# Optimization experiments

Hardware: AMD Instinct MI355X
Metric: run time of the kernel (lower is better)

## Reference

```python
import jax, jax.numpy as jnp
import numpy as np

N_GRAPHS = 100
NODES_PER_GRAPH = 1000
N = N_GRAPHS * NODES_PER_GRAPH
DEG = 16
E = N * DEG
IN_FEATS = 64
HIDDEN = 128
READOUT_DIM = HIDDEN // 2
SLOPE = 0.01
EPS = 1e-5


def leaky(x):
    return jnp.where(x >= 0, x, SLOPE * x)


def _kaiming(k, shape):
    # torch kaiming_uniform_, fan_in mode, leaky_relu gain
    fan_in = shape[0]
    gain = np.sqrt(2.0 / (1.0 + SLOPE ** 2))
    bound = gain * np.sqrt(3.0 / fan_in)
    return jax.random.uniform(k, shape, jnp.float32, -bound, bound)


def setup_inputs() -> dict:
    key = jax.random.key(0)
    ks = jax.random.split(key, 16)
    node_feats = jax.random.normal(ks[0], (N, IN_FEATS), jnp.float32)
    # within-graph random edges (batched graph of equal-sized components)
    src_local = jax.random.randint(ks[1], (E,), 0, NODES_PER_GRAPH)
    dst_local = jax.random.randint(ks[2], (E,), 0, NODES_PER_GRAPH)
    edge_graph = jnp.repeat(jnp.arange(N_GRAPHS, dtype=jnp.int32), E // N_GRAPHS)
    src = (edge_graph * NODES_PER_GRAPH + src_local).astype(jnp.int32)
    dst = (edge_graph * NODES_PER_GRAPH + dst_local).astype(jnp.int32)
    edge_weights = jax.random.uniform(ks[3], (E,), jnp.float32)
    node_graph = jnp.repeat(jnp.arange(N_GRAPHS, dtype=jnp.int32), NODES_PER_GRAPH)
    return {
        "node_feats": node_feats,
        "edge_weights": edge_weights,
        "W1": _kaiming(ks[4], (IN_FEATS, HIDDEN)),
        "W2": _kaiming(ks[5], (HIDDEN, HIDDEN)),
        "gn1_alpha": jnp.ones((HIDDEN,), jnp.float32),
        "gn1_gamma": jnp.ones((HIDDEN,), jnp.float32),
        "gn1_beta": jnp.zeros((HIDDEN,), jnp.float32),
        "gn2_alpha": jnp.ones((HIDDEN,), jnp.float32),
        "gn2_gamma": jnp.ones((HIDDEN,), jnp.float32),
        "gn2_beta": jnp.zeros((HIDDEN,), jnp.float32),
        "r1_w1": _kaiming(ks[6], (HIDDEN, HIDDEN)),
        "r1_b1": jnp.zeros((HIDDEN,), jnp.float32),
        "r1_w2": _kaiming(ks[7], (HIDDEN, READOUT_DIM)),
        "r1_b2": jnp.zeros((READOUT_DIM,), jnp.float32),
        "r2_w1": _kaiming(ks[8], (HIDDEN, HIDDEN)),
        "r2_b1": jnp.zeros((HIDDEN,), jnp.float32),
        "r2_w2": _kaiming(ks[9], (HIDDEN, READOUT_DIM)),
        "r2_b2": jnp.zeros((READOUT_DIM,), jnp.float32),
        "src": src,
        "dst": dst,
        "node_graph": node_graph,
    }


def _graph_conv(x, W, src, dst, ew, out_isqrt, in_isqrt):
    # DGL GraphConv norm='both', no bias: D_in^{-1/2} A_w D_out^{-1/2} X W
    h = (x * out_isqrt[:, None]) @ W                 # [N, out]
    m = h[src] * ew[:, None]                         # [E, out] gather + edge weight
    agg = jax.ops.segment_sum(m, dst, num_segments=N)  # scatter-add
    return agg * in_isqrt[:, None]


def _graph_norm(x, alpha, gamma, beta, node_graph, inv_cnt):
    mean = jax.ops.segment_sum(x, node_graph, num_segments=N_GRAPHS) * inv_cnt
    sub = x - alpha * mean[node_graph]
    var = jax.ops.segment_sum(sub * sub, node_graph, num_segments=N_GRAPHS) * inv_cnt
    return gamma * sub / jnp.sqrt(var[node_graph] + EPS) + beta


def _readout(x, w1, b1, w2, b2, node_graph, inv_cnt):
    # deep-sets style universal readout: rho(mean(phi(h_v)))
    h = leaky(x @ w1 + b1)
    pooled = jax.ops.segment_sum(h, node_graph, num_segments=N_GRAPHS) * inv_cnt
    return leaky(pooled @ w2 + b2)


def reference(node_feats, edge_weights, W1, W2,
              gn1_alpha, gn1_gamma, gn1_beta,
              gn2_alpha, gn2_gamma, gn2_beta,
              r1_w1, r1_b1, r1_w2, r1_b2,
              r2_w1, r2_b1, r2_w2, r2_b2,
              src, dst, node_graph):
    ones_e = jnp.ones((E,), jnp.float32)
    out_deg = jnp.clip(jax.ops.segment_sum(ones_e, src, num_segments=N), 1.0)
    in_deg = jnp.clip(jax.ops.segment_sum(ones_e, dst, num_segments=N), 1.0)
    out_isqrt = jax.lax.rsqrt(out_deg)
    in_isqrt = jax.lax.rsqrt(in_deg)
    inv_cnt = 1.0 / NODES_PER_GRAPH

    h = _graph_conv(node_feats, W1, src, dst, edge_weights, out_isqrt, in_isqrt)
    h = leaky(_graph_norm(h, gn1_alpha, gn1_gamma, gn1_beta, node_graph, inv_cnt))
    # dropout is identity in eval mode
    r1 = _readout(h, r1_w1, r1_b1, r1_w2, r1_b2, node_graph, inv_cnt)
    m1 = jax.ops.segment_sum(h, node_graph, num_segments=N_GRAPHS) * inv_cnt

    h = _graph_conv(h, W2, src, dst, edge_weights, out_isqrt, in_isqrt)
    h = leaky(_graph_norm(h, gn2_alpha, gn2_gamma, gn2_beta, node_graph, inv_cnt))
    r2 = _readout(h, r2_w1, r2_b1, r2_w2, r2_b2, node_graph, inv_cnt)
    m2 = jax.ops.segment_sum(h, node_graph, num_segments=N_GRAPHS) * inv_cnt

    readout = jnp.concatenate([r1, m1, r2, m2], axis=1)  # [G, 2*H + 2*H/2] = [100, 384]
    return leaky(readout)
```

## Files before the change

kernel.cpp:

```cpp
#include <hip/hip_runtime.h>
#include <cstddef>
#include <cstdint>

#define NG   100
#define NPG  1000
#define NN   (NG * NPG)
#define NE   (NN * 16)
#define EPG  (NE / NG)
#define CSRG 40000
#define MINREC 20
#define FIN  64
#define HID  128
#define RD   64
#define SLOPE 0.01f
#define EPSV  1e-5f
#define NSTRIP 250
#define GSN   40

using short8 = __attribute__((ext_vector_type(8))) short;
using f32x4  = __attribute__((ext_vector_type(4))) float;
typedef unsigned short u16;

__device__ __forceinline__ float leaky(float x) { return x >= 0.f ? x : SLOPE * x; }

__device__ __forceinline__ u16 f2bf(float f) {
  union { float f; unsigned u; } v; v.f = f;
  return (u16)((v.u + 0x7fffu + ((v.u >> 16) & 1u)) >> 16);
}
__device__ __forceinline__ float bf2f(u16 u) {
  union { unsigned u; float f; } v; v.u = ((unsigned)u) << 16;
  return v.f;
}

__device__ __forceinline__ bool swz(int b, int per_g, int& g, int& part) {
  const int xcd = b & 7;
  const int slot = b >> 3;
  g = xcd + 8 * (slot / per_g);
  part = slot % per_g;
  return g < NG;
}

__global__ __launch_bounds__(256) void wt_k(const float* __restrict__ W1,
                                            const float* __restrict__ W2,
                                            const float* __restrict__ R1,
                                            const float* __restrict__ R2,
                                            u16* __restrict__ Wt1,
                                            u16* __restrict__ Wt2,
                                            u16* __restrict__ Rt1,
                                            u16* __restrict__ Rt2) {
  const int idx = blockIdx.x * 256 + threadIdx.x;
  if (idx < FIN * HID) {
    const int n = idx >> 6, k = idx & 63;
    Wt1[idx] = f2bf(W1[k * HID + n]);
  } else {
    const int j = idx - FIN * HID;
    const int m = j >> 14, r = j & 16383;
    const int n = r >> 7, k = r & 127;
    const float* s = (m == 0) ? W2 : (m == 1) ? R1 : R2;
    u16* d = (m == 0) ? Wt2 : (m == 1) ? Rt1 : Rt2;
    d[r] = f2bf(s[k * HID + n]);
  }
}

__global__ __launch_bounds__(1024) void build_k(const int* __restrict__ src,
                                                const int* __restrict__ dst,
                                                const float* __restrict__ ew,
                                                int* __restrict__ cin_,
                                                int* __restrict__ cout_,
                                                int* __restrict__ offs,
                                                unsigned* __restrict__ csr) {
  __shared__ int hin[NPG];
  __shared__ int hout[NPG];
  __shared__ int cur[NPG];
  __shared__ int wtot[16];
  int g, part;
  if (!swz(blockIdx.x, 1, g, part)) return;
  const int t = threadIdx.x;
  const int lane = t & 63, wave = t >> 6;
  const int nb = g * NPG, eb = g * EPG;
  if (t < NPG) { hin[t] = 0; hout[t] = 0; }
  __syncthreads();
  for (int e = t; e < EPG; e += 4096) {
    int s4[4], d4[4];
#pragma unroll
    for (int k = 0; k < 4; ++k) {
      const int ee = e + k * 1024;
      if (ee < EPG) { s4[k] = src[eb + ee]; d4[k] = dst[eb + ee]; }
      else d4[k] = -1;
    }
#pragma unroll
    for (int k = 0; k < 4; ++k)
      if (d4[k] >= 0) {
        atomicAdd(&hout[s4[k] - nb], 1);
        atomicAdd(&hin[d4[k] - nb], 1);
      }
  }
  __syncthreads();
  int v[4], vr[4];
  int loc = 0;
#pragma unroll
  for (int k = 0; k < 4; ++k) {
    const int idx = t * 4 + k;
    v[k] = (idx < NPG) ? hin[idx] : 0;
    const int c4 = (v[k] + 3) & ~3;
    vr[k] = (idx < NPG) ? ((c4 > MINREC) ? c4 : MINREC) : 0;
    loc += vr[k];
  }
  int incl = loc;
#pragma unroll
  for (int d = 1; d < 64; d <<= 1) {
    const int x = __shfl_up(incl, d);
    if (lane >= d) incl += x;
  }
  if (lane == 63) wtot[wave] = incl;
  if (t < NPG) { cin_[nb + t] = hin[t]; cout_[nb + t] = hout[t]; }
  __syncthreads();
  int wexc = 0;
  for (int i = 0; i < wave; ++i) wexc += wtot[i];
  int run = g * CSRG + wexc + (incl - loc);
#pragma unroll
  for (int k = 0; k < 4; ++k) {
    const int idx = t * 4 + k;
    if (idx < NPG) {
      offs[nb + idx] = run;
      cur[idx] = run;
      for (int z = v[k]; z < vr[k]; ++z) csr[run + z] = 0;
      run += vr[k];
    }
  }
  __syncthreads();
  for (int e = t; e < EPG; e += 4096) {
    int s4[4], d4[4]; float w4[4];
#pragma unroll
    for (int k = 0; k < 4; ++k) {
      const int ee = e + k * 1024;
      if (ee < EPG) { s4[k] = src[eb + ee]; d4[k] = dst[eb + ee]; w4[k] = ew[eb + ee]; }
      else d4[k] = -1;
    }
#pragma unroll
    for (int k = 0; k < 4; ++k)
      if (d4[k] >= 0) {
        const int pos = atomicAdd(&cur[d4[k] - nb], 1);
        csr[pos] = ((unsigned)(s4[k] - nb) << 16) | (unsigned)f2bf(w4[k]);
      }
  }
}

__global__ __launch_bounds__(256) void gemm1_k(const float* __restrict__ X,
                                               const u16* __restrict__ Wt,
                                               const int* __restrict__ cout_,
                                               u16* __restrict__ Y) {
  __shared__ u16 Xl[64 * FIN];
  __shared__ u16 Wl[HID * FIN];
  const int tid = threadIdx.x;
  const int wave = tid >> 6, lane = tid & 63, l15 = lane & 15, quad = lane >> 4;
  int g, part;
  if (!swz(blockIdx.x, 4, g, part)) return;
  const int base = g * NPG + part * NSTRIP;
  const int kq = tid & 15;
  const int srow = tid >> 4;

  for (int i = tid; i < HID * (FIN / 8); i += 256) {
    const int n = i >> 3, c = i & 7;
    const short8 w = *(const short8*)(Wt + n * FIN + c * 8);
    *(short8*)&Wl[n * FIN + ((c ^ (n & 7)) << 3)] = w;
  }
  float4 xpre[4];
#pragma unroll
  for (int it = 0; it < 4; ++it) {
    const int rowi = srow + it * 16;
    xpre[it] = (rowi < NSTRIP) ? *(const float4*)(X + (size_t)(base + rowi) * FIN + kq * 4)
                               : make_float4(0.f, 0.f, 0.f, 0.f);
  }
  for (int pass = 0; pass < 4; ++pass) {
    __syncthreads();
#pragma unroll
    for (int it = 0; it < 4; ++it) {
      const int r = srow + it * 16;
      ushort4 u = make_ushort4(f2bf(xpre[it].x), f2bf(xpre[it].y),
                               f2bf(xpre[it].z), f2bf(xpre[it].w));
      const int c = kq >> 1, half = kq & 1;
      *(ushort4*)&Xl[r * FIN + (((c ^ (r & 7)) << 3) | (half << 2))] = u;
    }
    __syncthreads();
    if (pass < 3) {
#pragma unroll
      for (int it = 0; it < 4; ++it) {
        const int rowi = (pass + 1) * 64 + srow + it * 16;
        xpre[it] = (rowi < NSTRIP) ? *(const float4*)(X + (size_t)(base + rowi) * FIN + kq * 4)
                                   : make_float4(0.f, 0.f, 0.f, 0.f);
      }
    }
    short8 a[2];
    const int arow = wave * 16 + l15;
#pragma unroll
    for (int kt = 0; kt < 2; ++kt)
      a[kt] = *(const short8*)&Xl[arow * FIN + (((kt * 4 + quad) ^ (l15 & 7)) << 3)];
    float sc[4];
    int rows[4];
#pragma unroll
    for (int r = 0; r < 4; ++r) {
      rows[r] = pass * 64 + wave * 16 + quad * 4 + r;
      sc[r] = (rows[r] < NSTRIP) ? rsqrtf(fmaxf((float)cout_[base + rows[r]], 1.0f)) : 0.f;
    }
#pragma unroll
    for (int ct = 0; ct < 8; ++ct) {
      f32x4 acc = {0.f, 0.f, 0.f, 0.f};
      const int brow = ct * 16 + l15;
#pragma unroll
      for (int kt = 0; kt < 2; ++kt) {
        const short8 b = *(const short8*)&Wl[brow * FIN + (((kt * 4 + quad) ^ (l15 & 7)) << 3)];
        acc = __builtin_amdgcn_mfma_f32_16x16x32_bf16(a[kt], b, acc, 0, 0, 0);
      }
      const int n = ct * 16 + l15;
#pragma unroll
      for (int r = 0; r < 4; ++r)
        if (rows[r] < NSTRIP) Y[(size_t)(base + rows[r]) * HID + n] = f2bf(acc[r] * sc[r]);
    }
  }
}

__device__ __forceinline__ void norm_affine(const float* sx, const float* sq,
                                            const float* alpha, const float* gamma,
                                            const float* beta, int g, int c8,
                                            float* Av, float* Bv) {
  const float inv = 1.0f / NPG;
#pragma unroll
  for (int j = 0; j < 8; ++j) {
    const int f = c8 * 8 + j;
    const float mean = sx[g * HID + f] * inv;
    const float ex2 = sq[g * HID + f] * inv;
    const float am = alpha[f] * mean;
    const float var = fmaxf(ex2 - 2.0f * am * mean + am * am, 0.0f);
    const float A = gamma[f] * rsqrtf(var + EPSV);
    Av[j] = A;
    Bv[j] = beta[f] - A * am;
  }
}

__global__ __launch_bounds__(256) void gemm_norm_k(const u16* __restrict__ Xb,
                                                   const u16* __restrict__ Wt,
                                                   const float* __restrict__ sx,
                                                   const float* __restrict__ sq,
                                                   const float* __restrict__ alpha,
                                                   const float* __restrict__ gamma,
                                                   const float* __restrict__ beta,
                                                   const int* __restrict__ cout_,
                                                   u16* __restrict__ Y) {
  __shared__ u16 Xl[64 * HID];
  __shared__ u16 Wl[HID * HID];
  const int tid = threadIdx.x;
  const int wave = tid >> 6, lane = tid & 63, l15 = lane & 15, quad = lane >> 4;
  int g, part;
  if (!swz(blockIdx.x, 4, g, part)) return;
  const int base = g * NPG + part * NSTRIP;
  const int c8 = tid & 15;
  const int srow = tid >> 4;

  for (int i = tid; i < HID * (HID / 8); i += 256) {
    const int n = i >> 4, c = i & 15;
    const short8 w = *(const short8*)(Wt + n * HID + c * 8);
    *(short8*)&Wl[n * HID + ((c ^ (n & 15)) << 3)] = w;
  }
  float Av[8], Bv[8];
  norm_affine(sx, sq, alpha, gamma, beta, g, c8, Av, Bv);
  const short8 z8 = {0, 0, 0, 0, 0, 0, 0, 0};
  short8 xpre[4];
#pragma unroll
  for (int it = 0; it < 4; ++it) {
    const int rowi = srow + it * 16;
    xpre[it] = (rowi < NSTRIP) ? *(const short8*)(Xb + (size_t)(base + rowi) * HID + c8 * 8) : z8;
  }
  for (int pass = 0; pass < 4; ++pass) {
    __syncthreads();
#pragma unroll
    for (int it = 0; it < 4; ++it) {
      const int r = srow + it * 16;
      const int rowi = pass * 64 + r;
      short8 o = z8;
      if (rowi < NSTRIP) {
#pragma unroll
        for (int j = 0; j < 8; ++j)
          o[j] = (short)f2bf(leaky(fmaf(Av[j], bf2f((u16)xpre[it][j]), Bv[j])));
      }
      *(short8*)&Xl[r * HID + ((c8 ^ (r & 15)) << 3)] = o;
    }
    __syncthreads();
    if (pass < 3) {
#pragma unroll
      for (int it = 0; it < 4; ++it) {
        const int rowi = (pass + 1) * 64 + srow + it * 16;
        xpre[it] = (rowi < NSTRIP) ? *(const short8*)(Xb + (size_t)(base + rowi) * HID + c8 * 8) : z8;
      }
    }
    short8 a[4];
    const int arow = wave * 16 + l15;
#pragma unroll
    for (int kt = 0; kt < 4; ++kt)
      a[kt] = *(const short8*)&Xl[arow * HID + (((kt * 4 + quad) ^ l15) << 3)];
    float sc[4];
    int rows[4];
#pragma unroll
    for (int r = 0; r < 4; ++r) {
      rows[r] = pass * 64 + wave * 16 + quad * 4 + r;
      sc[r] = (rows[r] < NSTRIP) ? rsqrtf(fmaxf((float)cout_[base + rows[r]], 1.0f)) : 0.f;
    }
#pragma unroll
    for (int ct = 0; ct < 8; ++ct) {
      f32x4 acc = {0.f, 0.f, 0.f, 0.f};
      const int brow = ct * 16 + l15;
#pragma unroll
      for (int kt = 0; kt < 4; ++kt) {
        const short8 b = *(const short8*)&Wl[brow * HID + (((kt * 4 + quad) ^ l15) << 3)];
        acc = __builtin_amdgcn_mfma_f32_16x16x32_bf16(a[kt], b, acc, 0, 0, 0);
      }
      const int n = ct * 16 + l15;
#pragma unroll
      for (int r = 0; r < 4; ++r)
        if (rows[r] < NSTRIP) Y[(size_t)(base + rows[r]) * HID + n] = f2bf(acc[r] * sc[r]);
    }
  }
}

struct RedT { float red[16][HID]; float hred[16][HID]; };
union ShT { u16 Xl[64 * HID]; RedT r; };

__global__ __launch_bounds__(256) void phi_pool_k(const u16* __restrict__ Xb,
                                                  const float* __restrict__ sx,
                                                  const float* __restrict__ sq,
                                                  const float* __restrict__ alpha,
                                                  const float* __restrict__ gamma,
                                                  const float* __restrict__ beta,
                                                  const u16* __restrict__ Wt,
                                                  const float* __restrict__ b1,
                                                  float* __restrict__ phi_sum,
                                                  float* __restrict__ h_sum) {
  __shared__ ShT sh;
  __shared__ u16 Wl[HID * HID];
  const int tid = threadIdx.x;
  const int wave = tid >> 6, lane = tid & 63, l15 = lane & 15, quad = lane >> 4;
  int g, part;
  if (!swz(blockIdx.x, 4, g, part)) return;
  const int base = g * NPG + part * NSTRIP;
  const int c8 = tid & 15;
  const int srow = tid >> 4;

  for (int i = tid; i < HID * (HID / 8); i += 256) {
    const int n = i >> 4, c = i & 15;
    const short8 w = *(const short8*)(Wt + n * HID + c * 8);
    *(short8*)&Wl[n * HID + ((c ^ (n & 15)) << 3)] = w;
  }
  float Av[8], Bv[8];
  norm_affine(sx, sq, alpha, gamma, beta, g, c8, Av, Bv);
  float bcol[8];
#pragma unroll
  for (int ct = 0; ct < 8; ++ct) bcol[ct] = b1[ct * 16 + l15];

  float pooled[8] = {0.f, 0.f, 0.f, 0.f, 0.f, 0.f, 0.f, 0.f};
  float hp[8] = {0.f, 0.f, 0.f, 0.f, 0.f, 0.f, 0.f, 0.f};
  const short8 z8 = {0, 0, 0, 0, 0, 0, 0, 0};
  short8 xpre[4];
#pragma unroll
  for (int it = 0; it < 4; ++it) {
    const int rowi = srow + it * 16;
    xpre[it] = (rowi < NSTRIP) ? *(const short8*)(Xb + (size_t)(base + rowi) * HID + c8 * 8) : z8;
  }
  for (int pass = 0; pass < 4; ++pass) {
    __syncthreads();
#pragma unroll
    for (int it = 0; it < 4; ++it) {
      const int r = srow + it * 16;
      const int rowi = pass * 64 + r;
      short8 o = z8;
      if (rowi < NSTRIP) {
#pragma unroll
        for (int j = 0; j < 8; ++j) {
          const float xn = leaky(fmaf(Av[j], bf2f((u16)xpre[it][j]), Bv[j]));
          hp[j] += xn;
          o[j] = (short)f2bf(xn);
        }
      }
      *(short8*)&sh.Xl[r * HID + ((c8 ^ (r & 15)) << 3)] = o;
    }
    __syncthreads();
    if (pass < 3) {
#pragma unroll
      for (int it = 0; it < 4; ++it) {
        const int rowi = (pass + 1) * 64 + srow + it * 16;
        xpre[it] = (rowi < NSTRIP) ? *(const short8*)(Xb + (size_t)(base + rowi) * HID + c8 * 8) : z8;
      }
    }
    short8 a[4];
    const int arow = wave * 16 + l15;
#pragma unroll
    for (int kt = 0; kt < 4; ++kt)
      a[kt] = *(const short8*)&sh.Xl[arow * HID + (((kt * 4 + quad) ^ l15) << 3)];
#pragma unroll
    for (int ct = 0; ct < 8; ++ct) {
      f32x4 acc = {0.f, 0.f, 0.f, 0.f};
      const int brow = ct * 16 + l15;
#pragma unroll
      for (int kt = 0; kt < 4; ++kt) {
        const short8 b = *(const short8*)&Wl[brow * HID + (((kt * 4 + quad) ^ l15) << 3)];
        acc = __builtin_amdgcn_mfma_f32_16x16x32_bf16(a[kt], b, acc, 0, 0, 0);
      }
#pragma unroll
      for (int r = 0; r < 4; ++r) {
        const int rowi = pass * 64 + wave * 16 + quad * 4 + r;
        if (rowi < NSTRIP) pooled[ct] += leaky(acc[r] + bcol[ct]);
      }
    }
  }
  __syncthreads();
  const int qi = wave * 4 + quad;
#pragma unroll
  for (int ct = 0; ct < 8; ++ct) sh.r.red[qi][ct * 16 + l15] = pooled[ct];
#pragma unroll
  for (int j = 0; j < 8; ++j) sh.r.hred[tid >> 4][(tid & 15) * 8 + j] = hp[j];
  __syncthreads();
  if (tid < HID) {
    float s = 0.f;
#pragma unroll
    for (int q = 0; q < 16; ++q) s += sh.r.red[q][tid];
    unsafeAtomicAdd(&phi_sum[g * HID + tid], s);
  } else {
    const int t = tid - HID;
    float s = 0.f;
#pragma unroll
    for (int rr = 0; rr < 16; ++rr) s += sh.r.hred[rr][t];
    unsafeAtomicAdd(&h_sum[g * HID + t], s);
  }
}

__global__ __launch_bounds__(256) void gather_k(const u16* __restrict__ H,
                                                const unsigned* __restrict__ csr,
                                                const int* __restrict__ offs,
                                                const int* __restrict__ cin_,
                                                u16* __restrict__ AGG,
                                                float* __restrict__ sx,
                                                float* __restrict__ sq) {
  __shared__ float redx[4][HID];
  __shared__ float redq[4][HID];
  const int wave = threadIdx.x >> 6;
  const int lane = threadIdx.x & 63;
  int g, part;
  if (!swz(blockIdx.x, 25, g, part)) return;
  const int nb = g * NPG;
  const int base = nb + part * GSN;
  const int loff = lane * 2;
  const u16* __restrict__ Hg = H + (size_t)nb * HID;

  float sxa = 0.f, sxb = 0.f, sqa = 0.f, sqb = 0.f;
  for (int it = 0; it < 3; ++it) {
    const int nc = (it < 2) ? 4 : 2;
    int nn[4], off[4], cnt[4], c4p[4];
    float isq[4];
    const uint4* p[4];
#pragma unroll
    for (int c = 0; c < 4; ++c) {
      const int j = it * 4 + c;
      const int node = base + wave + ((j < 10) ? j : 0) * 4;
      nn[c] = node;
      const int nu = __builtin_amdgcn_readfirstlane(node);
      off[c] = __builtin_amdgcn_readfirstlane(offs[nu]);
      cnt[c] = (c < nc) ? __builtin_amdgcn_readfirstlane(cin_[nu]) : 0;
      const int cr = (cnt[c] + 3) & ~3;
      c4p[c] = ((cr > MINREC) ? cr : MINREC) >> 2;
      isq[c] = rsqrtf(fmaxf((float)cnt[c], 1.0f));
      p[c] = (const uint4*)__builtin_assume_aligned(csr + off[c], 16);
    }
    float ax[4] = {0.f, 0.f, 0.f, 0.f};
    float ay[4] = {0.f, 0.f, 0.f, 0.f};
#pragma unroll
    for (int t = 0; t < 5; ++t) {
      uint4 r[4];
      unsigned u[4][4];
#pragma unroll
      for (int c = 0; c < 4; ++c)
        if (c < nc) {
          r[c] = p[c][t];
          u[c][0] = *(const unsigned*)(Hg + (size_t)(r[c].x >> 16) * HID + loff);
          u[c][1] = *(const unsigned*)(Hg + (size_t)(r[c].y >> 16) * HID + loff);
          u[c][2] = *(const unsigned*)(Hg + (size_t)(r[c].z >> 16) * HID + loff);
          u[c][3] = *(const unsigned*)(Hg + (size_t)(r[c].w >> 16) * HID + loff);
        }
#pragma unroll
      for (int c = 0; c < 4; ++c)
        if (c < nc) {
          const float w0 = bf2f((u16)(r[c].x & 0xffffu));
          const float w1 = bf2f((u16)(r[c].y & 0xffffu));
          const float w2 = bf2f((u16)(r[c].z & 0xffffu));
          const float w3 = bf2f((u16)(r[c].w & 0xffffu));
          ax[c] = fmaf(w0, __uint_as_float(u[c][0] << 16), ax[c]);
          ay[c] = fmaf(w0, __uint_as_float(u[c][0] & 0xffff0000u), ay[c]);
          ax[c] = fmaf(w1, __uint_as_float(u[c][1] << 16), ax[c]);
          ay[c] = fmaf(w1, __uint_as_float(u[c][1] & 0xffff0000u), ay[c]);
          ax[c] = fmaf(w2, __uint_as_float(u[c][2] << 16), ax[c]);
          ay[c] = fmaf(w2, __uint_as_float(u[c][2] & 0xffff0000u), ay[c]);
          ax[c] = fmaf(w3, __uint_as_float(u[c][3] << 16), ax[c]);
          ay[c] = fmaf(w3, __uint_as_float(u[c][3] & 0xffff0000u), ay[c]);
        }
    }
#pragma unroll
    for (int c = 0; c < 4; ++c) {
      for (int t = 5; t < c4p[c]; ++t) {
        const uint4 r = p[c][t];
        const unsigned u0 = *(const unsigned*)(Hg + (size_t)(r.x >> 16) * HID + loff);
        const unsigned u1 = *(const unsigned*)(Hg + (size_t)(r.y >> 16) * HID + loff);
        const unsigned u2 = *(const unsigned*)(Hg + (size_t)(r.z >> 16) * HID + loff);
        const unsigned u3 = *(const unsigned*)(Hg + (size_t)(r.w >> 16) * HID + loff);
        const float w0 = bf2f((u16)(r.x & 0xffffu));
        const float w1 = bf2f((u16)(r.y & 0xffffu));
        const float w2 = bf2f((u16)(r.z & 0xffffu));
        const float w3 = bf2f((u16)(r.w & 0xffffu));
        ax[c] = fmaf(w0, __uint_as_float(u0 << 16), ax[c]);
        ay[c] = fmaf(w0, __uint_as_float(u0 & 0xffff0000u), ay[c]);
        ax[c] = fmaf(w1, __uint_as_float(u1 << 16), ax[c]);
        ay[c] = fmaf(w1, __uint_as_float(u1 & 0xffff0000u), ay[c]);
        ax[c] = fmaf(w2, __uint_as_float(u2 << 16), ax[c]);
        ay[c] = fmaf(w2, __uint_as_float(u2 & 0xffff0000u), ay[c]);
        ax[c] = fmaf(w3, __uint_as_float(u3 << 16), ax[c]);
        ay[c] = fmaf(w3, __uint_as_float(u3 & 0xffff0000u), ay[c]);
      }
    }
#pragma unroll
    for (int c = 0; c < 4; ++c)
      if (c < nc) {
        const float rx = ax[c] * isq[c];
        const float ry = ay[c] * isq[c];
        *(unsigned*)(AGG + (size_t)nn[c] * HID + loff) =
            (unsigned)f2bf(rx) | ((unsigned)f2bf(ry) << 16);
        sxa += rx; sxb += ry;
        sqa += rx * rx; sqb += ry * ry;
      }
  }
  redx[wave][loff] = sxa; redx[wave][loff + 1] = sxb;
  redq[wave][loff] = sqa; redq[wave][loff + 1] = sqb;
  __syncthreads();
  const int tid = threadIdx.x;
  if (tid < HID) {
    unsafeAtomicAdd(&sx[g * HID + tid],
                    redx[0][tid] + redx[1][tid] + redx[2][tid] + redx[3][tid]);
  } else {
    const int t = tid - HID;
    unsafeAtomicAdd(&sq[g * HID + t],
                    redq[0][t] + redq[1][t] + redq[2][t] + redq[3][t]);
  }
}

__global__ __launch_bounds__(64) void finalize_k(const float* __restrict__ phi_sum,
                                                 const float* __restrict__ h_sum,
                                                 const float* __restrict__ w2,
                                                 const float* __restrict__ b2,
                                                 float* __restrict__ out,
                                                 int roff, int moff) {
  const int g = blockIdx.x;
  const int j = threadIdx.x;
  float acc = b2[j];
#pragma unroll 8
  for (int k = 0; k < HID; ++k)
    acc += (phi_sum[g * HID + k] * (1.0f / NPG)) * w2[k * RD + j];
  const float r = leaky(acc);
  out[g * 384 + roff + j] = leaky(r);
  out[g * 384 + moff + j] = leaky(h_sum[g * HID + j] * (1.0f / NPG));
  out[g * 384 + moff + 64 + j] = leaky(h_sum[g * HID + 64 + j] * (1.0f / NPG));
}

extern "C" void kernel_launch(void* const* d_in, const int* in_sizes, int n_in,
                              void* d_out, int out_size, void* d_ws, size_t ws_size,
                              hipStream_t stream) {
  const float* node_feats = (const float*)d_in[0];
  const float* ew   = (const float*)d_in[1];
  const float* W1   = (const float*)d_in[2];
  const float* W2   = (const float*)d_in[3];
  const float* g1a  = (const float*)d_in[4];
  const float* g1g  = (const float*)d_in[5];
  const float* g1b  = (const float*)d_in[6];
  const float* g2a  = (const float*)d_in[7];
  const float* g2g  = (const float*)d_in[8];
  const float* g2b  = (const float*)d_in[9];
  const float* r1w1 = (const float*)d_in[10];
  const float* r1b1 = (const float*)d_in[11];
  const float* r1w2 = (const float*)d_in[12];
  const float* r1b2 = (const float*)d_in[13];
  const float* r2w1 = (const float*)d_in[14];
  const float* r2b1 = (const float*)d_in[15];
  const float* r2w2 = (const float*)d_in[16];
  const float* r2b2 = (const float*)d_in[17];
  const int* src = (const int*)d_in[18];
  const int* dst = (const int*)d_in[19];
  float* out = (float*)d_out;

  char* wsb = (char*)d_ws;
  float* ps1     = (float*)wsb;
  float* hs1     = ps1 + NG * HID;
  float* ps2     = hs1 + NG * HID;
  float* hs2     = ps2 + NG * HID;
  float* sx1     = hs2 + NG * HID;
  float* sq1     = sx1 + NG * HID;
  float* sx2     = sq1 + NG * HID;
  float* sq2     = sx2 + NG * HID;
  int*   cin     = (int*)(sq2 + NG * HID);
  int*   cout_   = cin + NN;
  int*   offs    = cout_ + NN;
  unsigned* csr  = (unsigned*)(offs + NN);
  u16*   Wt1     = (u16*)(csr + (size_t)NG * CSRG);
  u16*   Wt2     = Wt1 + HID * FIN;
  u16*   Rt1     = Wt2 + HID * HID;
  u16*   Rt2     = Rt1 + HID * HID;
  u16*   bufA    = Rt2 + HID * HID;
  u16*   bufB    = bufA + (size_t)NN * HID;

  hipMemsetAsync(d_ws, 0, (size_t)(8 * NG * HID) * sizeof(float), stream);

  wt_k<<<(FIN * HID + 3 * HID * HID) / 256, 256, 0, stream>>>(
      W1, W2, r1w1, r2w1, Wt1, Wt2, Rt1, Rt2);
  build_k<<<8 * 13, 1024, 0, stream>>>(src, dst, ew, cin, cout_, offs, csr);

  const int gemm_grid = 8 * 4 * 13;
  const int gather_grid = 8 * 25 * 13;

  gemm1_k<<<gemm_grid, 256, 0, stream>>>(node_feats, Wt1, cout_, bufA);
  gather_k<<<gather_grid, 256, 0, stream>>>(bufA, csr, offs, cin, bufB, sx1, sq1);
  phi_pool_k<<<gemm_grid, 256, 0, stream>>>(bufB, sx1, sq1, g1a, g1g, g1b,
                                            Rt1, r1b1, ps1, hs1);
  finalize_k<<<NG, 64, 0, stream>>>(ps1, hs1, r1w2, r1b2, out, 0, 64);

  gemm_norm_k<<<gemm_grid, 256, 0, stream>>>(bufB, Wt2, sx1, sq1, g1a, g1g, g1b,
                                             cout_, bufA);
  gather_k<<<gather_grid, 256, 0, stream>>>(bufA, csr, offs, cin, bufB, sx2, sq2);
  phi_pool_k<<<gemm_grid, 256, 0, stream>>>(bufB, sx2, sq2, g2a, g2g, g2b,
                                            Rt2, r2b1, ps2, hs2);
  finalize_k<<<NG, 64, 0, stream>>>(ps2, hs2, r2w2, r2b2, out, 192, 256);
}
```

Before: 294.2 us.

## Fuse preprocessing, CSR build and first GEMM into one front kernel; merge phi-pool with next GEMM

```diff
diff --git a/kernel.cpp b/kernel.cpp
--- a/kernel.cpp
+++ b/kernel.cpp
@@ -40,182 +40,166 @@
   return g < NG;
 }
 
-__global__ __launch_bounds__(256) void wt_k(const float* __restrict__ W1,
-                                            const float* __restrict__ W2,
-                                            const float* __restrict__ R1,
-                                            const float* __restrict__ R2,
-                                            u16* __restrict__ Wt1,
-                                            u16* __restrict__ Wt2,
-                                            u16* __restrict__ Rt1,
-                                            u16* __restrict__ Rt2) {
-  const int idx = blockIdx.x * 256 + threadIdx.x;
-  if (idx < FIN * HID) {
-    const int n = idx >> 6, k = idx & 63;
-    Wt1[idx] = f2bf(W1[k * HID + n]);
-  } else {
-    const int j = idx - FIN * HID;
-    const int m = j >> 14, r = j & 16383;
-    const int n = r >> 7, k = r & 127;
-    const float* s = (m == 0) ? W2 : (m == 1) ? R1 : R2;
-    u16* d = (m == 0) ? Wt2 : (m == 1) ? Rt1 : Rt2;
-    d[r] = f2bf(s[k * HID + n]);
-  }
-}
-
-__global__ __launch_bounds__(1024) void build_k(const int* __restrict__ src,
-                                                const int* __restrict__ dst,
-                                                const float* __restrict__ ew,
-                                                int* __restrict__ cin_,
-                                                int* __restrict__ cout_,
-                                                int* __restrict__ offs,
-                                                unsigned* __restrict__ csr) {
-  __shared__ int hin[NPG];
-  __shared__ int hout[NPG];
-  __shared__ int cur[NPG];
-  __shared__ int wtot[16];
+struct BldSh { int hin[NPG]; int hout[NPG]; int cur[NPG]; int wtot[16]; };
+struct GemSh { u16 Xl[64 * FIN]; u16 W[HID * FIN]; };
+union FrontSh { BldSh b; GemSh g; };
+
+__global__ __launch_bounds__(1024) void front_k(
+    const float* __restrict__ X0, const float* __restrict__ ew,
+    const int* __restrict__ src, const int* __restrict__ dst,
+    const float* __restrict__ W1, const float* __restrict__ W2f,
+    const float* __restrict__ R1f, const float* __restrict__ R2f,
+    u16* __restrict__ Wt2, u16* __restrict__ Rt1, u16* __restrict__ Rt2,
+    int* __restrict__ cin_, int* __restrict__ offs,
+    unsigned* __restrict__ csr, u16* __restrict__ bufA,
+    float* __restrict__ zeroreg) {
+  __shared__ FrontSh u;
+  const int b = blockIdx.x;
+  const int t = threadIdx.x;
+  if (b >= 208) {
+    const int idx = (b - 208) * 1024 + t;
+    if (idx < 3 * HID * HID) {
+      const int m = idx >> 14, r = idx & 16383;
+      const int n = r >> 7, k = r & 127;
+      const float* s = (m == 0) ? W2f : (m == 1) ? R1f : R2f;
+      u16* d = (m == 0) ? Wt2 : (m == 1) ? Rt1 : Rt2;
+      d[r] = f2bf(s[k * HID + n]);
+    }
+    if (idx < (8 * NG * HID) / 4)
+      ((float4*)zeroreg)[idx] = make_float4(0.f, 0.f, 0.f, 0.f);
+    return;
+  }
   int g, part;
-  if (!swz(blockIdx.x, 1, g, part)) return;
-  const int t = threadIdx.x;
+  if (!swz(b, 2, g, part)) return;
   const int lane = t & 63, wave = t >> 6;
   const int nb = g * NPG, eb = g * EPG;
-  if (t < NPG) { hin[t] = 0; hout[t] = 0; }
-  __syncthreads();
-  for (int e = t; e < EPG; e += 4096) {
-    int s4[4], d4[4];
+
+  if (part == 0) {
+    if (t < NPG) { u.b.hin[t] = 0; u.b.hout[t] = 0; }
+    __syncthreads();
+    for (int e = t; e < EPG; e += 4096) {
+      int s4[4], d4[4];
+#pragma unroll
+      for (int k = 0; k < 4; ++k) {
+        const int ee = e + k * 1024;
+        if (ee < EPG) { s4[k] = src[eb + ee]; d4[k] = dst[eb + ee]; }
+        else d4[k] = -1;
+      }
+#pragma unroll
+      for (int k = 0; k < 4; ++k)
+        if (d4[k] >= 0) {
+          atomicAdd(&u.b.hout[s4[k] - nb], 1);
+          atomicAdd(&u.b.hin[d4[k] - nb], 1);
+        }
+    }
+    __syncthreads();
+    float* houtf = (float*)u.b.hout;
+    if (t < NPG) {
+      const int c = u.b.hout[t];
+      houtf[t] = rsqrtf((float)(c > 0 ? c : 1));
+    }
+    int v[4], vr[4];
+    int loc = 0;
 #pragma unroll
     for (int k = 0; k < 4; ++k) {
-      const int ee = e + k * 1024;
-      if (ee < EPG) { s4[k] = src[eb + ee]; d4[k] = dst[eb + ee]; }
-      else d4[k] = -1;
-    }
-#pragma unroll
-    for (int k = 0; k < 4; ++k)
-      if (d4[k] >= 0) {
-        atomicAdd(&hout[s4[k] - nb], 1);
-        atomicAdd(&hin[d4[k] - nb], 1);
-      }
-  }
-  __syncthreads();
-  int v[4], vr[4];
-  int loc = 0;
-#pragma unroll
-  for (int k = 0; k < 4; ++k) {
-    const int idx = t * 4 + k;
-    v[k] = (idx < NPG) ? hin[idx] : 0;
-    const int c4 = (v[k] + 3) & ~3;
-    vr[k] = (idx < NPG) ? ((c4 > MINREC) ? c4 : MINREC) : 0;
-    loc += vr[k];
-  }
-  int incl = loc;
-#pragma unroll
-  for (int d = 1; d < 64; d <<= 1) {
-    const int x = __shfl_up(incl, d);
-    if (lane >= d) incl += x;
-  }
-  if (lane == 63) wtot[wave] = incl;
-  if (t < NPG) { cin_[nb + t] = hin[t]; cout_[nb + t] = hout[t]; }
-  __syncthreads();
-  int wexc = 0;
-  for (int i = 0; i < wave; ++i) wexc += wtot[i];
-  int run = g * CSRG + wexc + (incl - loc);
-#pragma unroll
-  for (int k = 0; k < 4; ++k) {
-    const int idx = t * 4 + k;
-    if (idx < NPG) {
-      offs[nb + idx] = run;
-      cur[idx] = run;
-      for (int z = v[k]; z < vr[k]; ++z) csr[run + z] = 0;
-      run += vr[k];
-    }
-  }
-  __syncthreads();
-  for (int e = t; e < EPG; e += 4096) {
-    int s4[4], d4[4]; float w4[4];
+      const int idx = t * 4 + k;
+      v[k] = (idx < NPG) ? u.b.hin[idx] : 0;
+      const int c4 = (v[k] + 3) & ~3;
+      vr[k] = (idx < NPG) ? ((c4 > MINREC) ? c4 : MINREC) : 0;
+      loc += vr[k];
+    }
+    int incl = loc;
+#pragma unroll
+    for (int d = 1; d < 64; d <<= 1) {
+      const int x = __shfl_up(incl, d);
+      if (lane >= d) incl += x;
+    }
+    if (lane == 63) u.b.wtot[wave] = incl;
+    if (t < NPG) cin_[nb + t] = u.b.hin[t];
+    __syncthreads();
+    int wexc = 0;
+    for (int i = 0; i < wave; ++i) wexc += u.b.wtot[i];
+    int run = g * CSRG + wexc + (incl - loc);
 #pragma unroll
     for (int k = 0; k < 4; ++k) {
-      const int ee = e + k * 1024;
-      if (ee < EPG) { s4[k] = src[eb + ee]; d4[k] = dst[eb + ee]; w4[k] = ew[eb + ee]; }
-      else d4[k] = -1;
-    }
-#pragma unroll
-    for (int k = 0; k < 4; ++k)
-      if (d4[k] >= 0) {
-        const int pos = atomicAdd(&cur[d4[k] - nb], 1);
-        csr[pos] = ((unsigned)(s4[k] - nb) << 16) | (unsigned)f2bf(w4[k]);
-      }
-  }
-}
-
-__global__ __launch_bounds__(256) void gemm1_k(const float* __restrict__ X,
-                                               const u16* __restrict__ Wt,
-                                               const int* __restrict__ cout_,
-                                               u16* __restrict__ Y) {
-  __shared__ u16 Xl[64 * FIN];
-  __shared__ u16 Wl[HID * FIN];
-  const int tid = threadIdx.x;
-  const int wave = tid >> 6, lane = tid & 63, l15 = lane & 15, quad = lane >> 4;
-  int g, part;
-  if (!swz(blockIdx.x, 4, g, part)) return;
-  const int base = g * NPG + part * NSTRIP;
-  const int kq = tid & 15;
-  const int srow = tid >> 4;
-
-  for (int i = tid; i < HID * (FIN / 8); i += 256) {
-    const int n = i >> 3, c = i & 7;
-    const short8 w = *(const short8*)(Wt + n * FIN + c * 8);
-    *(short8*)&Wl[n * FIN + ((c ^ (n & 7)) << 3)] = w;
-  }
-  float4 xpre[4];
-#pragma unroll
-  for (int it = 0; it < 4; ++it) {
-    const int rowi = srow + it * 16;
-    xpre[it] = (rowi < NSTRIP) ? *(const float4*)(X + (size_t)(base + rowi) * FIN + kq * 4)
-                               : make_float4(0.f, 0.f, 0.f, 0.f);
-  }
-  for (int pass = 0; pass < 4; ++pass) {
+      const int idx = t * 4 + k;
+      if (idx < NPG) {
+        offs[nb + idx] = run;
+        u.b.cur[idx] = run;
+        for (int z = v[k]; z < vr[k]; ++z) csr[run + z] = 0;
+        run += vr[k];
+      }
+    }
     __syncthreads();
-#pragma unroll
-    for (int it = 0; it < 4; ++it) {
-      const int r = srow + it * 16;
-      ushort4 u = make_ushort4(f2bf(xpre[it].x), f2bf(xpre[it].y),
-                               f2bf(xpre[it].z), f2bf(xpre[it].w));
-      const int c = kq >> 1, half = kq & 1;
-      *(ushort4*)&Xl[r * FIN + (((c ^ (r & 7)) << 3) | (half << 2))] = u;
-    }
-    __syncthreads();
-    if (pass < 3) {
-#pragma unroll
-      for (int it = 0; it < 4; ++it) {
-        const int rowi = (pass + 1) * 64 + srow + it * 16;
-        xpre[it] = (rowi < NSTRIP) ? *(const float4*)(X + (size_t)(base + rowi) * FIN + kq * 4)
-                                   : make_float4(0.f, 0.f, 0.f, 0.f);
-      }
-    }
-    short8 a[2];
-    const int arow = wave * 16 + l15;
-#pragma unroll
-    for (int kt = 0; kt < 2; ++kt)
-      a[kt] = *(const short8*)&Xl[arow * FIN + (((kt * 4 + quad) ^ (l15 & 7)) << 3)];
-    float sc[4];
-    int rows[4];
-#pragma unroll
-    for (int r = 0; r < 4; ++r) {
-      rows[r] = pass * 64 + wave * 16 + quad * 4 + r;
-      sc[r] = (rows[r] < NSTRIP) ? rsqrtf(fmaxf((float)cout_[base + rows[r]], 1.0f)) : 0.f;
-    }
-#pragma unroll
-    for (int ct = 0; ct < 8; ++ct) {
-      f32x4 acc = {0.f, 0.f, 0.f, 0.f};
-      const int brow = ct * 16 + l15;
-#pragma unroll
-      for (int kt = 0; kt < 2; ++kt) {
-        const short8 b = *(const short8*)&Wl[brow * FIN + (((kt * 4 + quad) ^ (l15 & 7)) << 3)];
-        acc = __builtin_amdgcn_mfma_f32_16x16x32_bf16(a[kt], b, acc, 0, 0, 0);
-      }
-      const int n = ct * 16 + l15;
-#pragma unroll
-      for (int r = 0; r < 4; ++r)
-        if (rows[r] < NSTRIP) Y[(size_t)(base + rows[r]) * HID + n] = f2bf(acc[r] * sc[r]);
+    for (int e = t; e < EPG; e += 4096) {
+      int s4[4], d4[4];
+      float w4[4];
+#pragma unroll
+      for (int k = 0; k < 4; ++k) {
+        const int ee = e + k * 1024;
+        if (ee < EPG) { s4[k] = src[eb + ee]; d4[k] = dst[eb + ee]; w4[k] = ew[eb + ee]; }
+        else d4[k] = -1;
+      }
+#pragma unroll
+      for (int k = 0; k < 4; ++k)
+        if (d4[k] >= 0) {
+          const int sl = s4[k] - nb;
+          const int pos = atomicAdd(&u.b.cur[d4[k] - nb], 1);
+          csr[pos] = ((unsigned)sl << 16) | (unsigned)f2bf(w4[k] * houtf[sl]);
+        }
+    }
+  } else {
+    const int l15 = lane & 15, quad = lane >> 4;
+    const int rg = wave >> 2, cg = wave & 3;
+    {
+      const int n = t & 127, ko = t >> 7;
+      short8 w8;
+#pragma unroll
+      for (int j = 0; j < 8; ++j) w8[j] = (short)f2bf(W1[(ko * 8 + j) * HID + n]);
+      *(short8*)&u.g.W[n * FIN + ((ko ^ (n & 7)) << 3)] = w8;
+    }
+    const int kq = t & 15, srow = t >> 4;
+    float4 xpre = (srow < NPG)
+        ? *(const float4*)(X0 + (size_t)(nb + srow) * FIN + kq * 4)
+        : make_float4(0.f, 0.f, 0.f, 0.f);
+    for (int pass = 0; pass < 16; ++pass) {
+      __syncthreads();
+      {
+        ushort4 uu = make_ushort4(f2bf(xpre.x), f2bf(xpre.y), f2bf(xpre.z), f2bf(xpre.w));
+        const int cc = kq >> 1, half = kq & 1;
+        *(ushort4*)&u.g.Xl[srow * FIN + (((cc ^ (srow & 7)) << 3) | (half << 2))] = uu;
+      }
+      __syncthreads();
+      if (pass < 15) {
+        const int rowi = (pass + 1) * 64 + srow;
+        xpre = (rowi < NPG)
+            ? *(const float4*)(X0 + (size_t)(nb + rowi) * FIN + kq * 4)
+            : make_float4(0.f, 0.f, 0.f, 0.f);
+      }
+      short8 a[2];
+      const int arow = rg * 16 + l15;
+#pragma unroll
+      for (int kt = 0; kt < 2; ++kt)
+        a[kt] = *(const short8*)&u.g.Xl[arow * FIN + (((kt * 4 + quad) ^ (l15 & 7)) << 3)];
+      int rows[4];
+#pragma unroll
+      for (int r = 0; r < 4; ++r) rows[r] = pass * 64 + rg * 16 + quad * 4 + r;
+#pragma unroll
+      for (int q2 = 0; q2 < 2; ++q2) {
+        const int ct = cg * 2 + q2;
+        f32x4 acc = {0.f, 0.f, 0.f, 0.f};
+        const int brow = ct * 16 + l15;
+#pragma unroll
+        for (int kt = 0; kt < 2; ++kt) {
+          const short8 bb = *(const short8*)&u.g.W[brow * FIN + (((kt * 4 + quad) ^ (l15 & 7)) << 3)];
+          acc = __builtin_amdgcn_mfma_f32_16x16x32_bf16(a[kt], bb, acc, 0, 0, 0);
+        }
+        const int n2 = ct * 16 + l15;
+#pragma unroll
+        for (int r = 0; r < 4; ++r)
+          if (rows[r] < NPG)
+            bufA[(size_t)(nb + rows[r]) * HID + n2] = f2bf(acc[r]);
+      }
     }
   }
 }
@@ -235,200 +219,6 @@
     const float A = gamma[f] * rsqrtf(var + EPSV);
     Av[j] = A;
     Bv[j] = beta[f] - A * am;
-  }
-}
-
-__global__ __launch_bounds__(256) void gemm_norm_k(const u16* __restrict__ Xb,
-                                                   const u16* __restrict__ Wt,
-                                                   const float* __restrict__ sx,
-                                                   const float* __restrict__ sq,
-                                                   const float* __restrict__ alpha,
-                                                   const float* __restrict__ gamma,
-                                                   const float* __restrict__ beta,
-                                                   const int* __restrict__ cout_,
-                                                   u16* __restrict__ Y) {
-  __shared__ u16 Xl[64 * HID];
-  __shared__ u16 Wl[HID * HID];
-  const int tid = threadIdx.x;
-  const int wave = tid >> 6, lane = tid & 63, l15 = lane & 15, quad = lane >> 4;
-  int g, part;
-  if (!swz(blockIdx.x, 4, g, part)) return;
-  const int base = g * NPG + part * NSTRIP;
-  const int c8 = tid & 15;
-  const int srow = tid >> 4;
-
-  for (int i = tid; i < HID * (HID / 8); i += 256) {
-    const int n = i >> 4, c = i & 15;
-    const short8 w = *(const short8*)(Wt + n * HID + c * 8);
-    *(short8*)&Wl[n * HID + ((c ^ (n & 15)) << 3)] = w;
-  }
-  float Av[8], Bv[8];
-  norm_affine(sx, sq, alpha, gamma, beta, g, c8, Av, Bv);
-  const short8 z8 = {0, 0, 0, 0, 0, 0, 0, 0};
-  short8 xpre[4];
-#pragma unroll
-  for (int it = 0; it < 4; ++it) {
-    const int rowi = srow + it * 16;
-    xpre[it] = (rowi < NSTRIP) ? *(const short8*)(Xb + (size_t)(base + rowi) * HID + c8 * 8) : z8;
-  }
-  for (int pass = 0; pass < 4; ++pass) {
-    __syncthreads();
-#pragma unroll
-    for (int it = 0; it < 4; ++it) {
-      const int r = srow + it * 16;
-      const int rowi = pass * 64 + r;
-      short8 o = z8;
-      if (rowi < NSTRIP) {
-#pragma unroll
-        for (int j = 0; j < 8; ++j)
-          o[j] = (short)f2bf(leaky(fmaf(Av[j], bf2f((u16)xpre[it][j]), Bv[j])));
-      }
-      *(short8*)&Xl[r * HID + ((c8 ^ (r & 15)) << 3)] = o;
-    }
-    __syncthreads();
-    if (pass < 3) {
-#pragma unroll
-      for (int it = 0; it < 4; ++it) {
-        const int rowi = (pass + 1) * 64 + srow + it * 16;
-        xpre[it] = (rowi < NSTRIP) ? *(const short8*)(Xb + (size_t)(base + rowi) * HID + c8 * 8) : z8;
-      }
-    }
-    short8 a[4];
-    const int arow = wave * 16 + l15;
-#pragma unroll
-    for (int kt = 0; kt < 4; ++kt)
-      a[kt] = *(const short8*)&Xl[arow * HID + (((kt * 4 + quad) ^ l15) << 3)];
-    float sc[4];
-    int rows[4];
-#pragma unroll
-    for (int r = 0; r < 4; ++r) {
-      rows[r] = pass * 64 + wave * 16 + quad * 4 + r;
-      sc[r] = (rows[r] < NSTRIP) ? rsqrtf(fmaxf((float)cout_[base + rows[r]], 1.0f)) : 0.f;
-    }
-#pragma unroll
-    for (int ct = 0; ct < 8; ++ct) {
-      f32x4 acc = {0.f, 0.f, 0.f, 0.f};
-      const int brow = ct * 16 + l15;
-#pragma unroll
-      for (int kt = 0; kt < 4; ++kt) {
-        const short8 b = *(const short8*)&Wl[brow * HID + (((kt * 4 + quad) ^ l15) << 3)];
-        acc = __builtin_amdgcn_mfma_f32_16x16x32_bf16(a[kt], b, acc, 0, 0, 0);
-      }
-      const int n = ct * 16 + l15;
-#pragma unroll
-      for (int r = 0; r < 4; ++r)
-        if (rows[r] < NSTRIP) Y[(size_t)(base + rows[r]) * HID + n] = f2bf(acc[r] * sc[r]);
-    }
-  }
-}
-
-struct RedT { float red[16][HID]; float hred[16][HID]; };
-union ShT { u16 Xl[64 * HID]; RedT r; };
-
-__global__ __launch_bounds__(256) void phi_pool_k(const u16* __restrict__ Xb,
-                                                  const float* __restrict__ sx,
-                                                  const float* __restrict__ sq,
-                                                  const float* __restrict__ alpha,
-                                                  const float* __restrict__ gamma,
-                                                  const float* __restrict__ beta,
-                                                  const u16* __restrict__ Wt,
-                                                  const float* __restrict__ b1,
-                                                  float* __restrict__ phi_sum,
-                                                  float* __restrict__ h_sum) {
-  __shared__ ShT sh;
-  __shared__ u16 Wl[HID * HID];
-  const int tid = threadIdx.x;
-  const int wave = tid >> 6, lane = tid & 63, l15 = lane & 15, quad = lane >> 4;
-  int g, part;
-  if (!swz(blockIdx.x, 4, g, part)) return;
-  const int base = g * NPG + part * NSTRIP;
-  const int c8 = tid & 15;
-  const int srow = tid >> 4;
-
-  for (int i = tid; i < HID * (HID / 8); i += 256) {
-    const int n = i >> 4, c = i & 15;
-    const short8 w = *(const short8*)(Wt + n * HID + c * 8);
-    *(short8*)&Wl[n * HID + ((c ^ (n & 15)) << 3)] = w;
-  }
-  float Av[8], Bv[8];
-  norm_affine(sx, sq, alpha, gamma, beta, g, c8, Av, Bv);
-  float bcol[8];
-#pragma unroll
-  for (int ct = 0; ct < 8; ++ct) bcol[ct] = b1[ct * 16 + l15];
-
-  float pooled[8] = {0.f, 0.f, 0.f, 0.f, 0.f, 0.f, 0.f, 0.f};
-  float hp[8] = {0.f, 0.f, 0.f, 0.f, 0.f, 0.f, 0.f, 0.f};
-  const short8 z8 = {0, 0, 0, 0, 0, 0, 0, 0};
-  short8 xpre[4];
-#pragma unroll
-  for (int it = 0; it < 4; ++it) {
-    const int rowi = srow + it * 16;
-    xpre[it] = (rowi < NSTRIP) ? *(const short8*)(Xb + (size_t)(base + rowi) * HID + c8 * 8) : z8;
-  }
-  for (int pass = 0; pass < 4; ++pass) {
-    __syncthreads();
-#pragma unroll
-    for (int it = 0; it < 4; ++it) {
-      const int r = srow + it * 16;
-      const int rowi = pass * 64 + r;
-      short8 o = z8;
-      if (rowi < NSTRIP) {
-#pragma unroll
-        for (int j = 0; j < 8; ++j) {
-          const float xn = leaky(fmaf(Av[j], bf2f((u16)xpre[it][j]), Bv[j]));
-          hp[j] += xn;
-          o[j] = (short)f2bf(xn);
-        }
-      }
-      *(short8*)&sh.Xl[r * HID + ((c8 ^ (r & 15)) << 3)] = o;
-    }
-    __syncthreads();
-    if (pass < 3) {
-#pragma unroll
-      for (int it = 0; it < 4; ++it) {
-        const int rowi = (pass + 1) * 64 + srow + it * 16;
-        xpre[it] = (rowi < NSTRIP) ? *(const short8*)(Xb + (size_t)(base + rowi) * HID + c8 * 8) : z8;
-      }
-    }
-    short8 a[4];
-    const int arow = wave * 16 + l15;
-#pragma unroll
-    for (int kt = 0; kt < 4; ++kt)
-      a[kt] = *(const short8*)&sh.Xl[arow * HID + (((kt * 4 + quad) ^ l15) << 3)];
-#pragma unroll
-    for (int ct = 0; ct < 8; ++ct) {
-      f32x4 acc = {0.f, 0.f, 0.f, 0.f};
-      const int brow = ct * 16 + l15;
-#pragma unroll
-      for (int kt = 0; kt < 4; ++kt) {
-        const short8 b = *(const short8*)&Wl[brow * HID + (((kt * 4 + quad) ^ l15) << 3)];
-        acc = __builtin_amdgcn_mfma_f32_16x16x32_bf16(a[kt], b, acc, 0, 0, 0);
-      }
-#pragma unroll
-      for (int r = 0; r < 4; ++r) {
-        const int rowi = pass * 64 + wave * 16 + quad * 4 + r;
-        if (rowi < NSTRIP) pooled[ct] += leaky(acc[r] + bcol[ct]);
-      }
-    }
-  }
-  __syncthreads();
-  const int qi = wave * 4 + quad;
-#pragma unroll
-  for (int ct = 0; ct < 8; ++ct) sh.r.red[qi][ct * 16 + l15] = pooled[ct];
-#pragma unroll
-  for (int j = 0; j < 8; ++j) sh.r.hred[tid >> 4][(tid & 15) * 8 + j] = hp[j];
-  __syncthreads();
-  if (tid < HID) {
-    float s = 0.f;
-#pragma unroll
-    for (int q = 0; q < 16; ++q) s += sh.r.red[q][tid];
-    unsafeAtomicAdd(&phi_sum[g * HID + tid], s);
-  } else {
-    const int t = tid - HID;
-    float s = 0.f;
-#pragma unroll
-    for (int rr = 0; rr < 16; ++rr) s += sh.r.hred[rr][t];
-    unsafeAtomicAdd(&h_sum[g * HID + t], s);
   }
 }
 
@@ -548,22 +338,163 @@
   }
 }
 
-__global__ __launch_bounds__(64) void finalize_k(const float* __restrict__ phi_sum,
-                                                 const float* __restrict__ h_sum,
-                                                 const float* __restrict__ w2,
-                                                 const float* __restrict__ b2,
-                                                 float* __restrict__ out,
-                                                 int roff, int moff) {
-  const int g = blockIdx.x;
+struct RedT { float red[16][HID]; float hred[16][HID]; };
+union ShT { u16 Xl[64 * HID]; RedT r; };
+
+template <bool DO_GEMM>
+__global__ __launch_bounds__(256) void phigemm_k(const u16* __restrict__ Xb,
+                                                 u16* __restrict__ Y,
+                                                 const u16* __restrict__ Wt,
+                                                 const u16* __restrict__ Rt,
+                                                 const float* __restrict__ sx,
+                                                 const float* __restrict__ sq,
+                                                 const float* __restrict__ alpha,
+                                                 const float* __restrict__ gamma,
+                                                 const float* __restrict__ beta,
+                                                 const float* __restrict__ b1,
+                                                 float* __restrict__ phi_sum,
+                                                 float* __restrict__ h_sum) {
+  __shared__ ShT sh;
+  __shared__ u16 Rl[HID * HID];
+  __shared__ u16 Wl[DO_GEMM ? HID * HID : 8];
+  const int tid = threadIdx.x;
+  const int wave = tid >> 6, lane = tid & 63, l15 = lane & 15, quad = lane >> 4;
+  int g, part;
+  if (!swz(blockIdx.x, 4, g, part)) return;
+  const int base = g * NPG + part * NSTRIP;
+  const int c8 = tid & 15;
+  const int srow = tid >> 4;
+
+  for (int i = tid; i < HID * (HID / 8); i += 256) {
+    const int n = i >> 4, c = i & 15;
+    const short8 r2 = *(const short8*)(Rt + n * HID + c * 8);
+    *(short8*)&Rl[n * HID + ((c ^ (n & 15)) << 3)] = r2;
+    if (DO_GEMM) {
+      const short8 w = *(const short8*)(Wt + n * HID + c * 8);
+      *(short8*)&Wl[n * HID + ((c ^ (n & 15)) << 3)] = w;
+    }
+  }
+  float Av[8], Bv[8];
+  norm_affine(sx, sq, alpha, gamma, beta, g, c8, Av, Bv);
+  float bcol[8];
+#pragma unroll
+  for (int ct = 0; ct < 8; ++ct) bcol[ct] = b1[ct * 16 + l15];
+
+  float pooled[8] = {0.f, 0.f, 0.f, 0.f, 0.f, 0.f, 0.f, 0.f};
+  float hp[8] = {0.f, 0.f, 0.f, 0.f, 0.f, 0.f, 0.f, 0.f};
+  const short8 z8 = {0, 0, 0, 0, 0, 0, 0, 0};
+  short8 xpre[4];
+#pragma unroll
+  for (int it = 0; it < 4; ++it) {
+    const int rowi = srow + it * 16;
+    xpre[it] = (rowi < NSTRIP) ? *(const short8*)(Xb + (size_t)(base + rowi) * HID + c8 * 8) : z8;
+  }
+  for (int pass = 0; pass < 4; ++pass) {
+    __syncthreads();
+#pragma unroll
+    for (int it = 0; it < 4; ++it) {
+      const int r = srow + it * 16;
+      const int rowi = pass * 64 + r;
+      short8 o = z8;
+      if (rowi < NSTRIP) {
+#pragma unroll
+        for (int j = 0; j < 8; ++j) {
+          const float xn = leaky(fmaf(Av[j], bf2f((u16)xpre[it][j]), Bv[j]));
+          hp[j] += xn;
+          o[j] = (short)f2bf(xn);
+        }
+      }
+      *(short8*)&sh.Xl[r * HID + ((c8 ^ (r & 15)) << 3)] = o;
+    }
+    __syncthreads();
+    if (pass < 3) {
+#pragma unroll
+      for (int it = 0; it < 4; ++it) {
+        const int rowi = (pass + 1) * 64 + srow + it * 16;
+        xpre[it] = (rowi < NSTRIP) ? *(const short8*)(Xb + (size_t)(base + rowi) * HID + c8 * 8) : z8;
+      }
+    }
+    short8 a[4];
+    const int arow = wave * 16 + l15;
+#pragma unroll
+    for (int kt = 0; kt < 4; ++kt)
+      a[kt] = *(const short8*)&sh.Xl[arow * HID + (((kt * 4 + quad) ^ l15) << 3)];
+    int rows[4];
+#pragma unroll
+    for (int r = 0; r < 4; ++r) rows[r] = pass * 64 + wave * 16 + quad * 4 + r;
+#pragma unroll
+    for (int ct = 0; ct < 8; ++ct) {
+      const int brow = ct * 16 + l15;
+      if (DO_GEMM) {
+        f32x4 accW = {0.f, 0.f, 0.f, 0.f};
+#pragma unroll
+        for (int kt = 0; kt < 4; ++kt) {
+          const short8 bb = *(const short8*)&Wl[brow * HID + (((kt * 4 + quad) ^ l15) << 3)];
+          accW = __builtin_amdgcn_mfma_f32_16x16x32_bf16(a[kt], bb, accW, 0, 0, 0);
+        }
+#pragma unroll
+        for (int r = 0; r < 4; ++r)
+          if (rows[r] < NSTRIP)
+            Y[(size_t)(base + rows[r]) * HID + ct * 16 + l15] = f2bf(accW[r]);
+      }
+      f32x4 accR = {0.f, 0.f, 0.f, 0.f};
+#pragma unroll
+      for (int kt = 0; kt < 4; ++kt) {
+        const short8 bb = *(const short8*)&Rl[brow * HID + (((kt * 4 + quad) ^ l15) << 3)];
+        accR = __builtin_amdgcn_mfma_f32_16x16x32_bf16(a[kt], bb, accR, 0, 0, 0);
+      }
+#pragma unroll
+      for (int r = 0; r < 4; ++r)
+        if (rows[r] < NSTRIP) pooled[ct] += leaky(accR[r] + bcol[ct]);
+    }
+  }
+  __syncthreads();
+  const int qi = wave * 4 + quad;
+#pragma unroll
+  for (int ct = 0; ct < 8; ++ct) sh.r.red[qi][ct * 16 + l15] = pooled[ct];
+#pragma unroll
+  for (int j = 0; j < 8; ++j) sh.r.hred[tid >> 4][(tid & 15) * 8 + j] = hp[j];
+  __syncthreads();
+  if (tid < HID) {
+    float s = 0.f;
+#pragma unroll
+    for (int q = 0; q < 16; ++q) s += sh.r.red[q][tid];
+    unsafeAtomicAdd(&phi_sum[g * HID + tid], s);
+  } else {
+    const int t = tid - HID;
+    float s = 0.f;
+#pragma unroll
+    for (int rr = 0; rr < 16; ++rr) s += sh.r.hred[rr][t];
+    unsafeAtomicAdd(&h_sum[g * HID + t], s);
+  }
+}
+
+__global__ __launch_bounds__(64) void fin_k(const float* __restrict__ ps1,
+                                            const float* __restrict__ hs1,
+                                            const float* __restrict__ ps2,
+                                            const float* __restrict__ hs2,
+                                            const float* __restrict__ r1w2,
+                                            const float* __restrict__ r1b2,
+                                            const float* __restrict__ r2w2,
+                                            const float* __restrict__ r2b2,
+                                            float* __restrict__ out) {
+  const int gb = blockIdx.x;
+  const bool L2 = gb >= NG;
+  const int g = L2 ? gb - NG : gb;
+  const float* ps = L2 ? ps2 : ps1;
+  const float* hs = L2 ? hs2 : hs1;
+  const float* w2 = L2 ? r2w2 : r1w2;
+  const float* b2 = L2 ? r2b2 : r1b2;
+  const int roff = L2 ? 192 : 0;
+  const int moff = L2 ? 256 : 64;
   const int j = threadIdx.x;
   float acc = b2[j];
 #pragma unroll 8
   for (int k = 0; k < HID; ++k)
-    acc += (phi_sum[g * HID + k] * (1.0f / NPG)) * w2[k * RD + j];
-  const float r = leaky(acc);
-  out[g * 384 + roff + j] = leaky(r);
-  out[g * 384 + moff + j] = leaky(h_sum[g * HID + j] * (1.0f / NPG));
-  out[g * 384 + moff + 64 + j] = leaky(h_sum[g * HID + 64 + j] * (1.0f / NPG));
+    acc += (ps[g * HID + k] * (1.0f / NPG)) * w2[k * RD + j];
+  out[g * 384 + roff + j] = leaky(leaky(acc));
+  out[g * 384 + moff + j] = leaky(hs[g * HID + j] * (1.0f / NPG));
+  out[g * 384 + moff + 64 + j] = leaky(hs[g * HID + 64 + j] * (1.0f / NPG));
 }
 
 extern "C" void kernel_launch(void* const* d_in, const int* in_sizes, int n_in,
@@ -601,35 +532,31 @@
   float* sx2     = sq1 + NG * HID;
   float* sq2     = sx2 + NG * HID;
   int*   cin     = (int*)(sq2 + NG * HID);
-  int*   cout_   = cin + NN;
-  int*   offs    = cout_ + NN;
+  int*   offs    = cin + NN;
   unsigned* csr  = (unsigned*)(offs + NN);
-  u16*   Wt1     = (u16*)(csr + (size_t)NG * CSRG);
-  u16*   Wt2     = Wt1 + HID * FIN;
+  u16*   Wt2     = (u16*)(csr + (size_t)NG * CSRG);
   u16*   Rt1     = Wt2 + HID * HID;
   u16*   Rt2     = Rt1 + HID * HID;
   u16*   bufA    = Rt2 + HID * HID;
   u16*   bufB    = bufA + (size_t)NN * HID;
 
-  hipMemsetAsync(d_ws, 0, (size_t)(8 * NG * HID) * sizeof(float), stream);
-
-  wt_k<<<(FIN * HID + 3 * HID * HID) / 256, 256, 0, stream>>>(
-      W1, W2, r1w1, r2w1, Wt1, Wt2, Rt1, Rt2);
-  build_k<<<8 * 13, 1024, 0, stream>>>(src, dst, ew, cin, cout_, offs, csr);
-
   const int gemm_grid = 8 * 4 * 13;
   const int gather_grid = 8 * 25 * 13;
 
-  gemm1_k<<<gemm_grid, 256, 0, stream>>>(node_feats, Wt1, cout_, bufA);
+  front_k<<<208 + 56, 1024, 0, stream>>>(node_feats, ew, src, dst,
+                                         W1, W2, r1w1, r2w1,
+                                         Wt2, Rt1, Rt2,
+                                         cin, offs, csr, bufA, ps1);
+
   gather_k<<<gather_grid, 256, 0, stream>>>(bufA, csr, offs, cin, bufB, sx1, sq1);
-  phi_pool_k<<<gemm_grid, 256, 0, stream>>>(bufB, sx1, sq1, g1a, g1g, g1b,
-                                            Rt1, r1b1, ps1, hs1);
-  finalize_k<<<NG, 64, 0, stream>>>(ps1, hs1, r1w2, r1b2, out, 0, 64);
-
-  gemm_norm_k<<<gemm_grid, 256, 0, stream>>>(bufB, Wt2, sx1, sq1, g1a, g1g, g1b,
-                                             cout_, bufA);
+  phigemm_k<true><<<gemm_grid, 256, 0, stream>>>(bufB, bufA, Wt2, Rt1,
+                                                 sx1, sq1, g1a, g1g, g1b,
+                                                 r1b1, ps1, hs1);
+
   gather_k<<<gather_grid, 256, 0, stream>>>(bufA, csr, offs, cin, bufB, sx2, sq2);
-  phi_pool_k<<<gemm_grid, 256, 0, stream>>>(bufB, sx2, sq2, g2a, g2g, g2b,
-                                            Rt2, r2b1, ps2, hs2);
-  finalize_k<<<NG, 64, 0, stream>>>(ps2, hs2, r2w2, r2b2, out, 192, 256);
-}
+  phigemm_k<false><<<gemm_grid, 256, 0, stream>>>(bufB, nullptr, nullptr, Rt2,
+                                                  sx2, sq2, g2a, g2g, g2b,
+                                                  r2b1, ps2, hs2);
+
+  fin_k<<<2 * NG, 64, 0, stream>>>(ps1, hs1, ps2, hs2, r1w2, r1b2, r2w2, r2b2, out);
+}
```

New measurement: 268.5 us. -8.8%, faster.
